# Kernel optimization log

Measured on AMD Instinct MI355X. Metric: run time of the kernel, lower is better.

## Reference

```python
import jax, jax.numpy as jnp
import numpy as np

B, N, L = 16, 512, 512          # batch, compound atoms, protein words
DIM = 10                         # compound feature dim
DM, H, DK, DFF = 128, 8, 16, 512 # transformer dims
LG, LO = 3, 3                    # layer_gnn, layer_output
NFP, NW = 10000, 10000           # vocab sizes
NEG = -9e15                      # GAT mask sentinel (matches torch code)


def _layernorm(x, g, b, eps=1e-6):
    # annotated-transformer LayerNorm: unbiased std, eps added to std
    m = jnp.mean(x, -1, keepdims=True)
    s = jnp.std(x, -1, keepdims=True, ddof=1)
    return g * (x - m) / (s + eps) + b


def _pos_encoding(length, d_model):
    pos = np.arange(length)[:, None]
    div = np.exp(np.arange(0, d_model, 2) * (-np.log(10000.0) / d_model))
    pe = np.zeros((length, d_model), np.float32)
    pe[:, 0::2] = np.sin(pos * div)
    pe[:, 1::2] = np.cos(pos * div)
    return jnp.asarray(pe)


def setup_inputs():
    ks = iter(jax.random.split(jax.random.key(0), 64))
    def nrm(shape, scale):
        return jax.random.normal(next(ks), shape, jnp.float32) * scale
    return dict(
        fingerprints=jax.random.randint(next(ks), (B, N), 0, NFP, jnp.int32),
        fp_mask=jnp.ones((B, N), jnp.float32),
        adjacency=jax.random.randint(next(ks), (B, N, N), 0, 2, jnp.int32),
        words=jax.random.randint(next(ks), (B, L), 0, NW, jnp.int32),
        words_mask=jnp.ones((B, L), jnp.float32),
        emb_fp=nrm((NFP, DIM), 0.1),
        emb_word=nrm((NW, DM), 0.1),
        Wg=nrm((LG, DIM, DIM), 0.3), bg=jnp.zeros((LG, DIM), jnp.float32),
        attn_a=nrm((LG, 2 * DIM), 0.3),
        Wq=nrm((DM, DM), 0.09), bq=jnp.zeros((DM,), jnp.float32),
        Wk=nrm((DM, DM), 0.09), bk=jnp.zeros((DM,), jnp.float32),
        Wv=nrm((DM, DM), 0.09), bv=jnp.zeros((DM,), jnp.float32),
        Wo=nrm((DM, DM), 0.09), bo=jnp.zeros((DM,), jnp.float32),
        ln1_g=jnp.ones((DM,), jnp.float32), ln1_b=jnp.zeros((DM,), jnp.float32),
        ln2_g=jnp.ones((DM,), jnp.float32), ln2_b=jnp.zeros((DM,), jnp.float32),
        lnf_g=jnp.ones((DM,), jnp.float32), lnf_b=jnp.zeros((DM,), jnp.float32),
        W1=nrm((DM, DFF), 0.09), b1=jnp.zeros((DFF,), jnp.float32),
        W2=nrm((DFF, DM), 0.045), b2=jnp.zeros((DM,), jnp.float32),
        Wtout=nrm((DM, DIM), 0.09), btout=jnp.zeros((DIM,), jnp.float32),
        Watt=nrm((DIM, DIM), 0.3), batt=jnp.zeros((DIM,), jnp.float32),
        Wout=nrm((LO, 2 * DIM, 2 * DIM), 0.2), bout=jnp.zeros((LO, 2 * DIM), jnp.float32),
        Wint=nrm((2 * DIM, 2), 0.2), bint=jnp.zeros((2,), jnp.float32),
    )


def _forward(fingerprints, fp_mask, adjacency, words, words_mask,
             emb_fp, emb_word, Wg, bg, attn_a,
             Wq, bq, Wk, bk, Wv, bv, Wo, bo,
             ln1_g, ln1_b, ln2_g, ln2_b, lnf_g, lnf_b,
             W1, b1, W2, b2, Wtout, btout,
             Watt, batt, Wout, bout, Wint, bint):
    # ---- GAT over compound graph (dropout disabled = eval/deterministic) ----
    xs = emb_fp[fingerprints]                     # [B,N,DIM]
    mask = fp_mask[:, :, None]                    # [B,N,1]
    adj = adjacency > 0
    for i in range(LG):
        h = jax.nn.relu(xs @ Wg[i] + bg[i]) * mask
        # e[b,i,j] = leaky_relu(a1.h_i + a2.h_j)  == leaky_relu([h_i||h_j] @ a)
        s1 = h @ attn_a[i, :DIM]                  # [B,N]
        s2 = h @ attn_a[i, DIM:]                  # [B,N]
        e = jax.nn.leaky_relu(s1[:, :, None] + s2[:, None, :])  # [B,N,N]
        att = jax.nn.softmax(jnp.where(adj, e, NEG), axis=2)
        xs = xs + att @ h
    compound = jnp.mean(xs * mask, axis=1, keepdims=True)       # [B,1,DIM]

    # ---- transformer encoder, 1 layer, annotated-transformer (pre-norm) ----
    x = emb_word[words] * jnp.sqrt(jnp.float32(DM)) + _pos_encoding(L, DM)
    m4 = words_mask[:, None, None, :] > 0         # [B,1,1,L]
    xn = _layernorm(x, ln1_g, ln1_b)
    heads = lambda t: t.reshape(B, L, H, DK).transpose(0, 2, 1, 3)
    q, k, v = heads(xn @ Wq + bq), heads(xn @ Wk + bk), heads(xn @ Wv + bv)
    scores = jnp.einsum('bhqd,bhkd->bhqk', q, k) / jnp.sqrt(jnp.float32(DK))
    p = jax.nn.softmax(jnp.where(m4, scores, -1e9), axis=-1)
    attn = jnp.einsum('bhqk,bhkd->bhqd', p, v).transpose(0, 2, 1, 3).reshape(B, L, DM)
    x = x + (attn @ Wo + bo)
    xn = _layernorm(x, ln2_g, ln2_b)
    x = x + (jax.nn.relu(xn @ W1 + b1) @ W2 + b2)
    x = _layernorm(x, lnf_g, lnf_b)
    word_vectors = jax.nn.relu(x) @ Wtout + btout  # [B,L,DIM]

    # ---- tanh cross-attention (attention_cnn) ----
    hc = jax.nn.relu(compound @ Watt + batt)       # [B,1,DIM]
    hp = jax.nn.relu(word_vectors @ Watt + batt)   # [B,L,DIM]
    w = jnp.tanh(jnp.einsum('bxd,bld->bxl', hc, hp))  # [B,1,L]
    protein = jnp.mean(w.transpose(0, 2, 1) * hp, axis=1, keepdims=True)  # [B,1,DIM]

    cat = jnp.concatenate([compound, protein], axis=2)  # [B,1,2*DIM]
    for j in range(LO):
        cat = jax.nn.relu(cat @ Wout[j] + bout[j])
    return jnp.squeeze(cat @ Wint + bint, axis=1)        # [B,2]


def reference(fingerprints, fp_mask, adjacency, words, words_mask,
              emb_fp, emb_word, Wg, bg, attn_a,
              Wq, bq, Wk, bk, Wv, bv, Wo, bo,
              ln1_g, ln1_b, ln2_g, ln2_b, lnf_g, lnf_b,
              W1, b1, W2, b2, Wtout, btout,
              Watt, batt, Wout, bout, Wint, bint):
    return _forward(fingerprints, fp_mask, adjacency, words, words_mask,
                    emb_fp, emb_word, Wg, bg, attn_a,
                    Wq, bq, Wk, bk, Wv, bv, Wo, bo,
                    ln1_g, ln1_b, ln2_g, ln2_b, lnf_g, lnf_b,
                    W1, b1, W2, b2, Wtout, btout,
                    Watt, batt, Wout, bout, Wint, bint)
```

## Files before the change

kernel.cpp:

```cpp
#include <hip/hip_runtime.h>
#include <hip/hip_bf16.h>
#include <math.h>

#define B 16
#define N 512
#define L 512
#define DIM 10
#define DM 128
#define H 8
#define DK 16
#define DFF 512
#define LG 3
#define LO 3
#define NEGV -9.0e15f
#define RF 16
#define AQR 64
#define RLOG2E 1.44269504f

__device__ __forceinline__ float wave_reduce_sum(float v) {
    #pragma unroll
    for (int o = 32; o > 0; o >>= 1) v += __shfl_down(v, o, 64);
    return v;
}

__device__ __forceinline__ float quad_sum(float x) {
    int y1 = __builtin_amdgcn_mov_dpp(__float_as_int(x), 0xB1, 0xF, 0xF, true);
    float s = x + __int_as_float(y1);
    int y2 = __builtin_amdgcn_mov_dpp(__float_as_int(s), 0x4E, 0xF, 0xF, true);
    return s + __int_as_float(y2);
}

__device__ __forceinline__ float half_reduce_sum(float v) {
    #pragma unroll
    for (int o = 16; o > 0; o >>= 1) v += __shfl_xor(v, o, 64);
    return v;
}

__device__ __forceinline__ float fast_exp2(float x) {
    return __builtin_amdgcn_exp2f(x);
}


__global__ void k_embed_fp(const int* __restrict__ fing, const float* __restrict__ emb_fp,
                           float* __restrict__ xs) {
    int idx = blockIdx.x * blockDim.x + threadIdx.x;
    if (idx >= B * N * DIM) return;
    int d = idx % DIM;
    int bn = idx / DIM;
    xs[idx] = emb_fp[fing[bn] * DIM + d];
}

__global__ void k_gnn_h(const float* __restrict__ xs, const float* __restrict__ fp_mask,
                        const float* __restrict__ Wg, const float* __restrict__ bg,
                        const float* __restrict__ aatt,
                        float* __restrict__ h, float* __restrict__ s1, float* __restrict__ s2) {
    int bn = blockIdx.x * blockDim.x + threadIdx.x;
    if (bn >= B * N) return;
    float x[DIM];
    #pragma unroll
    for (int d = 0; d < DIM; d++) x[d] = xs[bn * DIM + d];
    float m = fp_mask[bn];
    float a1 = 0.f, a2 = 0.f;
    #pragma unroll
    for (int j = 0; j < DIM; j++) {
        float acc = bg[j];
        #pragma unroll
        for (int d = 0; d < DIM; d++) acc += x[d] * Wg[d * DIM + j];
        acc = fmaxf(acc, 0.f) * m;
        h[bn * DIM + j] = acc;
        a1 += acc * aatt[j];
        a2 += acc * aatt[DIM + j];
    }
    s1[bn] = a1;
    s2[bn] = a2;
}

__global__ void k_gnn_att(const float* __restrict__ h, const float* __restrict__ s1,
                          const float* __restrict__ s2, const int* __restrict__ adj,
                          float* __restrict__ xs) {
    int b  = blockIdx.x / (N / 16);
    int rg = blockIdx.x % (N / 16);
    int t = threadIdx.x;
    int g  = t >> 4;
    int ll = t & 15;
    int i = rg * 16 + g;

    __shared__ float h_s[N * DIM];
    __shared__ float s2_s[N];

    const float* hb = h + (long)b * N * DIM;
    for (int idx = t; idx < N * DIM; idx += 256) h_s[idx] = hb[idx];
    for (int j = t; j < N; j += 256) s2_s[j] = s2[b * N + j];
    __syncthreads();

    float s1v = s1[b * N + i];
    const int* adjrow = adj + ((long)b * N + i) * N;

    float sum = 0.f;
    float a[DIM];
    #pragma unroll
    for (int d = 0; d < DIM; d++) a[d] = 0.f;
    #pragma unroll
    for (int c = 0; c < 32; c++) {
        int j = c * 16 + ll;
        float xsc = s1v + s2_s[j];
        xsc = xsc > 0.f ? xsc : 0.01f * xsc;
        float e = (adjrow[j] > 0) ? xsc : NEGV;
        float p = fast_exp2(e * RLOG2E);
        sum += p;
        #pragma unroll
        for (int d = 0; d < DIM; d++) a[d] += p * h_s[j * DIM + d];
    }
    #pragma unroll
    for (int off = 1; off < 16; off <<= 1) {
        sum += __shfl_xor(sum, off, 64);
        #pragma unroll
        for (int d = 0; d < DIM; d++) a[d] += __shfl_xor(a[d], off, 64);
    }
    if (ll < DIM) {
        float av = a[0];
        if (ll == 1) av = a[1]; else if (ll == 2) av = a[2]; else if (ll == 3) av = a[3];
        else if (ll == 4) av = a[4]; else if (ll == 5) av = a[5]; else if (ll == 6) av = a[6];
        else if (ll == 7) av = a[7]; else if (ll == 8) av = a[8]; else if (ll == 9) av = a[9];
        xs[((long)b * N + i) * DIM + ll] += av / sum;
    }
}

__global__ void k_compound(const float* __restrict__ xs, const float* __restrict__ fp_mask,
                           const float* __restrict__ Watt, const float* __restrict__ batt,
                           float* __restrict__ compound, float* __restrict__ hc) {
    int b = blockIdx.x;
    int t = threadIdx.x;
    int wid = t >> 6, lane = t & 63;
    float lacc[DIM];
    #pragma unroll
    for (int d = 0; d < DIM; d++) lacc[d] = 0.f;
    for (int n = t; n < N; n += 256) {
        float m = fp_mask[b * N + n];
        #pragma unroll
        for (int d = 0; d < DIM; d++) lacc[d] += xs[((long)b * N + n) * DIM + d] * m;
    }
    __shared__ float red[4][DIM];
    __shared__ float comp_s[DIM];
    #pragma unroll
    for (int d = 0; d < DIM; d++) lacc[d] = wave_reduce_sum(lacc[d]);
    if (lane == 0) {
        #pragma unroll
        for (int d = 0; d < DIM; d++) red[wid][d] = lacc[d];
    }
    __syncthreads();
    if (t < DIM) {
        float c = (red[0][t] + red[1][t] + red[2][t] + red[3][t]) / (float)N;
        compound[b * DIM + t] = c;
        comp_s[t] = c;
    }
    __syncthreads();
    if (t < DIM) {
        float acc = batt[t];
        #pragma unroll
        for (int e = 0; e < DIM; e++) acc += comp_s[e] * Watt[e * DIM + t];
        hc[b * DIM + t] = fmaxf(acc, 0.f);
    }
}


__global__ void k_pe(float* __restrict__ pe) {
    int idx = blockIdx.x * blockDim.x + threadIdx.x;
    if (idx >= L * DM) return;
    int d = idx % DM, l = idx / DM;
    int k = d >> 1;
    double div = exp((double)(2 * k) * (-log(10000.0) / (double)DM));
    double ang = (double)l * div;
    pe[idx] = (d & 1) ? (float)cos(ang) : (float)sin(ang);
}

__global__ void k_embed_ln(const int* __restrict__ words, const float* __restrict__ emb,
                           const float* __restrict__ pe, const float* __restrict__ g,
                           const float* __restrict__ bb,
                           float* __restrict__ x, float* __restrict__ xn) {
    int row = blockIdx.x;
    int t = threadIdx.x;
    int wid = t >> 6, lane = t & 63;
    int l = row % L;
    float v = emb[(long)words[row] * DM + t] * sqrtf(128.0f) + pe[l * DM + t];
    x[(long)row * DM + t] = v;
    float s = wave_reduce_sum(v);
    __shared__ float r2[2], r3[2];
    if (lane == 0) r2[wid] = s;
    __syncthreads();
    float mean = (r2[0] + r2[1]) / (float)DM;
    float dv = v - mean;
    float q = wave_reduce_sum(dv * dv);
    if (lane == 0) r3[wid] = q;
    __syncthreads();
    float sd = sqrtf((r3[0] + r3[1]) / (float)(DM - 1)) + 1e-6f;
    xn[(long)row * DM + t] = g[t] * dv / sd + bb[t];
}

__global__ void k_qkv(const float* __restrict__ xn,
                      const float* __restrict__ Wq, const float* __restrict__ bq,
                      const float* __restrict__ Wk, const float* __restrict__ bk,
                      const float* __restrict__ Wv, const float* __restrict__ bv,
                      float* __restrict__ q, float* __restrict__ k, float* __restrict__ v) {
    long row0 = (long)blockIdx.x * RF;
    int t = threadIdx.x;
    __shared__ float xs_s[RF * DM];
    for (int i = t; i < RF * DM; i += 384) xs_s[i] = xn[row0 * DM + i];
    __syncthreads();
    int proj = t / DM;
    int j = t % DM;
    const float* W    = proj == 0 ? Wq : (proj == 1 ? Wk : Wv);
    const float* bias = proj == 0 ? bq : (proj == 1 ? bk : bv);
    float* out        = proj == 0 ? q  : (proj == 1 ? k  : v);
    float acc[RF];
    #pragma unroll
    for (int r = 0; r < RF; r++) acc[r] = bias[j];
    for (int d4 = 0; d4 < DM / 4; d4++) {
        float w0 = W[(4 * d4 + 0) * DM + j];
        float w1 = W[(4 * d4 + 1) * DM + j];
        float w2 = W[(4 * d4 + 2) * DM + j];
        float w3 = W[(4 * d4 + 3) * DM + j];
        #pragma unroll
        for (int r = 0; r < RF; r++) {
            float4 xv = ((const float4*)&xs_s[r * DM])[d4];
            acc[r] += xv.x * w0 + xv.y * w1 + xv.z * w2 + xv.w * w3;
        }
    }
    #pragma unroll
    for (int r = 0; r < RF; r++) {
        long row = row0 + r;
        int b = (int)(row / L), l = (int)(row % L);
        out[(((long)b * H + j / DK) * L + l) * DK + (j % DK)] = acc[r];
    }
}

__global__ void __launch_bounds__(256, 4)
k_attn(const float* __restrict__ q, const float* __restrict__ k,
       const float* __restrict__ v, const float* __restrict__ wmask,
       float* __restrict__ attnout) {
    int blk = blockIdx.x;
    int qc = blk % (L / AQR);
    int bh = blk / (L / AQR);
    int b = bh / H, hh = bh % H;
    int t = threadIdx.x;
    int sl = t & 3;
    int r = t >> 2;
    int l = qc * AQR + r;

    __shared__ float4 k_s[L * 4];
    __shared__ float wm_s[L];
    const float4* kb4 = (const float4*)(k + (long)bh * L * DK);
    for (int i = t; i < L * 4; i += 256) k_s[i] = kb4[i];
    for (int j = t; j < L; j += 256) wm_s[j] = (wmask[b * L + j] > 0.f) ? 0.f : -1.443e9f;
    __syncthreads();

    float4 qr = ((const float4*)(q + ((long)bh * L + l) * DK))[sl];
    const float qsc = 0.25f * RLOG2E;
    qr.x *= qsc; qr.y *= qsc; qr.z *= qsc; qr.w *= qsc;

    const float4* vb4 = (const float4*)(v + (long)bh * L * DK);

    float ssum = 0.f;
    float4 acc = make_float4(0.f, 0.f, 0.f, 0.f);

    for (int c = 0; c < L / 8; c++) {
        int j0 = c * 8;
        float s8[8];
        #pragma unroll
        for (int jj = 0; jj < 8; jj++) {
            float4 kk = k_s[(j0 + jj) * 4 + sl];
            float part = qr.x * kk.x + qr.y * kk.y + qr.z * kk.z + qr.w * kk.w;
            s8[jj] = quad_sum(part);
        }
        const float4* mp = (const float4*)&wm_s[j0];
        float4 ma = mp[0], mb = mp[1];
        s8[0] += ma.x; s8[1] += ma.y; s8[2] += ma.z; s8[3] += ma.w;
        s8[4] += mb.x; s8[5] += mb.y; s8[6] += mb.z; s8[7] += mb.w;

        #pragma unroll
        for (int jj = 0; jj < 8; jj++) {
            float p = fast_exp2(s8[jj]);
            ssum += p;
            float4 vv = vb4[(j0 + jj) * 4 + sl];
            acc.x += p * vv.x; acc.y += p * vv.y; acc.z += p * vv.z; acc.w += p * vv.w;
        }
    }

    float inv = 1.f / ssum;
    float4* outp = (float4*)(attnout + ((long)b * L + l) * DM + hh * DK);
    outp[sl] = make_float4(acc.x * inv, acc.y * inv, acc.z * inv, acc.w * inv);
}

__global__ void k_oproj(const float* __restrict__ attnout, const float* __restrict__ Wo,
                        const float* __restrict__ bo, float* __restrict__ x) {
    long row0 = (long)blockIdx.x * RF;
    int t = threadIdx.x;
    __shared__ float a_s[RF * DM];
    for (int i = t; i < RF * DM; i += 128) a_s[i] = attnout[row0 * DM + i];
    __syncthreads();
    float acc[RF];
    #pragma unroll
    for (int r = 0; r < RF; r++) acc[r] = bo[t];
    for (int d4 = 0; d4 < DM / 4; d4++) {
        float w0 = Wo[(4 * d4 + 0) * DM + t];
        float w1 = Wo[(4 * d4 + 1) * DM + t];
        float w2 = Wo[(4 * d4 + 2) * DM + t];
        float w3 = Wo[(4 * d4 + 3) * DM + t];
        #pragma unroll
        for (int r = 0; r < RF; r++) {
            float4 av = ((const float4*)&a_s[r * DM])[d4];
            acc[r] += av.x * w0 + av.y * w1 + av.z * w2 + av.w * w3;
        }
    }
    #pragma unroll
    for (int r = 0; r < RF; r++) x[(row0 + r) * DM + t] += acc[r];
}

__global__ void k_ffn_fused(const float* __restrict__ x,
                            const float* __restrict__ ln2_g, const float* __restrict__ ln2_b,
                            const float* __restrict__ W1, const float* __restrict__ b1,
                            const float* __restrict__ W2, const float* __restrict__ b2,
                            const float* __restrict__ lnf_g, const float* __restrict__ lnf_b,
                            const float* __restrict__ Wtout, const float* __restrict__ btout,
                            const float* __restrict__ Watt, const float* __restrict__ batt,
                            float* __restrict__ hp) {
    long row0 = (long)blockIdx.x * RF;
    int t = threadIdx.x;

    __shared__ float x_s[RF][DM];
    __shared__ float xn_s[RF][DM];
    __shared__ float h_s[RF][DFF];
    __shared__ float r_s[RF][DM + 4];
    __shared__ float wt_s[DM * DIM];
    __shared__ float wa_s[DIM * DIM];
    __shared__ float bt_s[DIM], ba_s[DIM];
    __shared__ float wv_s[RF][DIM];

    {
        float4 xv = ((const float4*)(x + row0 * DM))[t];
        ((float4*)&x_s[0][0])[t] = xv;
        for (int i = t; i < DM * DIM; i += 512) wt_s[i] = Wtout[i];
        for (int i = t; i < DIM * DIM; i += 512) wa_s[i] = Watt[i];
        if (t < DIM) { bt_s[t] = btout[t]; ba_s[t] = batt[t]; }
    }
    __syncthreads();

    {
        int row = t >> 5, c = t & 31;
        float4 v = ((const float4*)&x_s[row][0])[c];
        float s = half_reduce_sum(v.x + v.y + v.z + v.w);
        float mean = s / (float)DM;
        float4 dv = make_float4(v.x - mean, v.y - mean, v.z - mean, v.w - mean);
        float q = half_reduce_sum(dv.x * dv.x + dv.y * dv.y + dv.z * dv.z + dv.w * dv.w);
        float sd = sqrtf(q / (float)(DM - 1)) + 1e-6f;
        const float4 g4 = ((const float4*)ln2_g)[c];
        const float4 b4 = ((const float4*)ln2_b)[c];
        ((float4*)&xn_s[row][0])[c] = make_float4(
            g4.x * dv.x / sd + b4.x, g4.y * dv.y / sd + b4.y,
            g4.z * dv.z / sd + b4.z, g4.w * dv.w / sd + b4.w);
    }
    __syncthreads();

    {
        float acc[RF];
        #pragma unroll
        for (int r = 0; r < RF; r++) acc[r] = b1[t];
        for (int d4 = 0; d4 < DM / 4; d4++) {
            float w0 = W1[(4 * d4 + 0) * DFF + t];
            float w1 = W1[(4 * d4 + 1) * DFF + t];
            float w2 = W1[(4 * d4 + 2) * DFF + t];
            float w3 = W1[(4 * d4 + 3) * DFF + t];
            #pragma unroll
            for (int r = 0; r < RF; r++) {
                float4 xv = ((const float4*)&xn_s[r][0])[d4];
                acc[r] += xv.x * w0 + xv.y * w1 + xv.z * w2 + xv.w * w3;
            }
        }
        #pragma unroll
        for (int r = 0; r < RF; r++) h_s[r][t] = fmaxf(acc[r], 0.f);
    }
    __syncthreads();

    {
        int col = t & 127, rq = t >> 7;
        float acc2[4];
        #pragma unroll
        for (int rr = 0; rr < 4; rr++) acc2[rr] = b2[col];
        for (int f4 = 0; f4 < DFF / 4; f4++) {
            float w0 = W2[(4 * f4 + 0) * DM + col];
            float w1 = W2[(4 * f4 + 1) * DM + col];
            float w2 = W2[(4 * f4 + 2) * DM + col];
            float w3 = W2[(4 * f4 + 3) * DM + col];
            #pragma unroll
            for (int rr = 0; rr < 4; rr++) {
                float4 hv = ((const float4*)&h_s[rq * 4 + rr][0])[f4];
                acc2[rr] += hv.x * w0 + hv.y * w1 + hv.z * w2 + hv.w * w3;
            }
        }
        __syncthreads();
        #pragma unroll
        for (int rr = 0; rr < 4; rr++) {
            int row = rq * 4 + rr;
            xn_s[row][col] = x_s[row][col] + acc2[rr];
        }
    }
    __syncthreads();

    {
        int row = t >> 5, c = t & 31;
        float4 v = ((const float4*)&xn_s[row][0])[c];
        float s = half_reduce_sum(v.x + v.y + v.z + v.w);
        float mean = s / (float)DM;
        float4 dv = make_float4(v.x - mean, v.y - mean, v.z - mean, v.w - mean);
        float q = half_reduce_sum(dv.x * dv.x + dv.y * dv.y + dv.z * dv.z + dv.w * dv.w);
        float sd = sqrtf(q / (float)(DM - 1)) + 1e-6f;
        const float4 g4 = ((const float4*)lnf_g)[c];
        const float4 b4 = ((const float4*)lnf_b)[c];
        r_s[row][4 * c + 0] = fmaxf(g4.x * dv.x / sd + b4.x, 0.f);
        r_s[row][4 * c + 1] = fmaxf(g4.y * dv.y / sd + b4.y, 0.f);
        r_s[row][4 * c + 2] = fmaxf(g4.z * dv.z / sd + b4.z, 0.f);
        r_s[row][4 * c + 3] = fmaxf(g4.w * dv.w / sd + b4.w, 0.f);
    }
    __syncthreads();

    if (t < RF * DIM) {
        int row = t / DIM, o = t % DIM;
        float acc = bt_s[o];
        for (int d = 0; d < DM; d++) acc += r_s[row][d] * wt_s[d * DIM + o];
        wv_s[row][o] = acc;
    }
    __syncthreads();

    if (t < RF * DIM) {
        int row = t / DIM, o = t % DIM;
        float acc = ba_s[o];
        #pragma unroll
        for (int e = 0; e < DIM; e++) acc += wv_s[row][e] * wa_s[e * DIM + o];
        hp[(row0 + row) * DIM + o] = fmaxf(acc, 0.f);
    }
}

__global__ void k_final(const float* __restrict__ hp, const float* __restrict__ hc,
                        const float* __restrict__ compound, const float* __restrict__ Wout,
                        const float* __restrict__ bout, const float* __restrict__ Wint,
                        const float* __restrict__ bint, float* __restrict__ out) {
    int b = blockIdx.x;
    int t = threadIdx.x;
    int wid = t >> 6, lane = t & 63;

    __shared__ float wout_s[LO * 2 * DIM * 2 * DIM];
    __shared__ float bout_s[LO * 2 * DIM];
    __shared__ float wint_s[2 * DIM * 2];
    __shared__ float bint_s[2];
    __shared__ float hc_s[DIM];
    __shared__ float red[4][DIM];
    __shared__ float cat_s[2 * DIM];
    __shared__ float tmp_s[2 * DIM];

    for (int i = t; i < LO * 2 * DIM * 2 * DIM; i += 256) wout_s[i] = Wout[i];
    for (int i = t; i < LO * 2 * DIM; i += 256) bout_s[i] = bout[i];
    for (int i = t; i < 2 * DIM * 2; i += 256) wint_s[i] = Wint[i];
    if (t < 2) bint_s[t] = bint[t];
    if (t < DIM) hc_s[t] = hc[b * DIM + t];
    __syncthreads();

    float lacc[DIM];
    #pragma unroll
    for (int e = 0; e < DIM; e++) lacc[e] = 0.f;
    for (int l = t; l < L; l += 256) {
        const float* hpl = hp + ((long)b * L + l) * DIM;
        float hv[DIM];
        float dot = 0.f;
        #pragma unroll
        for (int e = 0; e < DIM; e++) { hv[e] = hpl[e]; dot += hc_s[e] * hv[e]; }
        float w = tanhf(dot);
        #pragma unroll
        for (int e = 0; e < DIM; e++) lacc[e] += w * hv[e];
    }
    #pragma unroll
    for (int e = 0; e < DIM; e++) lacc[e] = wave_reduce_sum(lacc[e]);
    if (lane == 0) {
        #pragma unroll
        for (int e = 0; e < DIM; e++) red[wid][e] = lacc[e];
    }
    __syncthreads();
    if (t < DIM) {
        cat_s[t] = compound[b * DIM + t];
        cat_s[DIM + t] = (red[0][t] + red[1][t] + red[2][t] + red[3][t]) / (float)L;
    }
    __syncthreads();

    for (int j = 0; j < LO; j++) {
        float acc = 0.f;
        if (t < 2 * DIM) {
            acc = bout_s[j * 2 * DIM + t];
            #pragma unroll
            for (int e = 0; e < 2 * DIM; e++)
                acc += cat_s[e] * wout_s[j * 2 * DIM * 2 * DIM + e * 2 * DIM + t];
            acc = fmaxf(acc, 0.f);
            tmp_s[t] = acc;
        }
        __syncthreads();
        if (t < 2 * DIM) cat_s[t] = tmp_s[t];
        __syncthreads();
    }
    if (t < 2) {
        float o = bint_s[t];
        #pragma unroll
        for (int e = 0; e < 2 * DIM; e++) o += cat_s[e] * wint_s[e * 2 + t];
        out[b * 2 + t] = o;
    }
}

extern "C" void kernel_launch(void* const* d_in, const int* in_sizes, int n_in,
                              void* d_out, int out_size, void* d_ws, size_t ws_size,
                              hipStream_t stream) {
    (void)in_sizes; (void)n_in; (void)out_size; (void)ws_size;
    const int*   fingerprints = (const int*)d_in[0];
    const float* fp_mask      = (const float*)d_in[1];
    const int*   adjacency    = (const int*)d_in[2];
    const int*   words        = (const int*)d_in[3];
    const float* words_mask   = (const float*)d_in[4];
    const float* emb_fp       = (const float*)d_in[5];
    const float* emb_word     = (const float*)d_in[6];
    const float* Wg   = (const float*)d_in[7];
    const float* bg   = (const float*)d_in[8];
    const float* attn_a = (const float*)d_in[9];
    const float* Wq = (const float*)d_in[10];
    const float* bq = (const float*)d_in[11];
    const float* Wk = (const float*)d_in[12];
    const float* bk = (const float*)d_in[13];
    const float* Wv = (const float*)d_in[14];
    const float* bv = (const float*)d_in[15];
    const float* Wo = (const float*)d_in[16];
    const float* bo = (const float*)d_in[17];
    const float* ln1_g = (const float*)d_in[18];
    const float* ln1_b = (const float*)d_in[19];
    const float* ln2_g = (const float*)d_in[20];
    const float* ln2_b = (const float*)d_in[21];
    const float* lnf_g = (const float*)d_in[22];
    const float* lnf_b = (const float*)d_in[23];
    const float* W1 = (const float*)d_in[24];
    const float* b1 = (const float*)d_in[25];
    const float* W2 = (const float*)d_in[26];
    const float* b2 = (const float*)d_in[27];
    const float* Wtout = (const float*)d_in[28];
    const float* btout = (const float*)d_in[29];
    const float* Watt  = (const float*)d_in[30];
    const float* batt  = (const float*)d_in[31];
    const float* Wout  = (const float*)d_in[32];
    const float* bout  = (const float*)d_in[33];
    const float* Wint  = (const float*)d_in[34];
    const float* bint  = (const float*)d_in[35];
    float* out = (float*)d_out;

    float* w = (float*)d_ws;
    float* xs = w;        w += B * N * DIM;
    float* h  = w;        w += B * N * DIM;
    float* s1 = w;        w += B * N;
    float* s2 = w;        w += B * N;
    float* compound = w;  w += B * DIM;
    float* hc = w;        w += B * DIM;
    float* pe = w;        w += L * DM;
    float* x  = w;        w += (long)B * L * DM;
    float* xn = w;        w += (long)B * L * DM;
    float* qb = w;        w += (long)B * H * L * DK;
    float* kb = w;        w += (long)B * H * L * DK;
    float* vb = w;        w += (long)B * H * L * DK;
    float* attnout = w;   w += (long)B * L * DM;
    float* hp = w;        w += (long)B * L * DIM;

    k_embed_fp<<<(B * N * DIM + 255) / 256, 256, 0, stream>>>(fingerprints, emb_fp, xs);
    for (int i = 0; i < LG; i++) {
        k_gnn_h<<<(B * N + 255) / 256, 256, 0, stream>>>(
            xs, fp_mask, Wg + i * DIM * DIM, bg + i * DIM, attn_a + i * 2 * DIM, h, s1, s2);
        k_gnn_att<<<B * (N / 16), 256, 0, stream>>>(h, s1, s2, adjacency, xs);
    }
    k_compound<<<B, 256, 0, stream>>>(xs, fp_mask, Watt, batt, compound, hc);

    k_pe<<<(L * DM + 255) / 256, 256, 0, stream>>>(pe);
    k_embed_ln<<<B * L, DM, 0, stream>>>(words, emb_word, pe, ln1_g, ln1_b, x, xn);
    k_qkv<<<B * L / RF, 3 * DM, 0, stream>>>(xn, Wq, bq, Wk, bk, Wv, bv, qb, kb, vb);
    k_attn<<<B * H * (L / AQR), 256, 0, stream>>>(qb, kb, vb, words_mask, attnout);
    k_oproj<<<B * L / RF, DM, 0, stream>>>(attnout, Wo, bo, x);
    k_ffn_fused<<<B * L / RF, DFF, 0, stream>>>(x, ln2_g, ln2_b, W1, b1, W2, b2,
                                                lnf_g, lnf_b, Wtout, btout, Watt, batt, hp);
    k_final<<<B, 256, 0, stream>>>(hp, hc, compound, Wout, bout, Wint, bint, out);
}
```

Before: 237.9 us.

## Split attention keys into two segments and merge partial sums in output projection

Attention blocks now each cover half of the key range (split-K), doubling the grid, and write unnormalised partial outputs plus row sums. The output projection then combines the two partials and normalises them. Separately, the fingerprint-embedding kernel is folded into the first GNN layer and the positional-encoding kernel is folded into the word-embedding LayerNorm kernel. The aim is more parallelism in attention and fewer launches, at the cost of extra partial-buffer traffic and per-thread double-precision sin/cos in the embedding kernel. The merge is valid only because the scores are never max-subtracted, so the softmax sums across segments combine directly.

```diff
diff --git a/kernel.cpp b/kernel.cpp
--- a/kernel.cpp
+++ b/kernel.cpp
@@ -15,6 +15,7 @@
 #define NEGV -9.0e15f
 #define RF 16
 #define AQR 64
+#define KSEG 256
 #define RLOG2E 1.44269504f
 
 __device__ __forceinline__ float wave_reduce_sum(float v) {
@@ -41,24 +42,23 @@
 }
 
 
-__global__ void k_embed_fp(const int* __restrict__ fing, const float* __restrict__ emb_fp,
-                           float* __restrict__ xs) {
-    int idx = blockIdx.x * blockDim.x + threadIdx.x;
-    if (idx >= B * N * DIM) return;
-    int d = idx % DIM;
-    int bn = idx / DIM;
-    xs[idx] = emb_fp[fing[bn] * DIM + d];
-}
-
-__global__ void k_gnn_h(const float* __restrict__ xs, const float* __restrict__ fp_mask,
+__global__ void k_gnn_h(const int* __restrict__ fing, const float* __restrict__ emb_fp,
+                        float* __restrict__ xs, const float* __restrict__ fp_mask,
                         const float* __restrict__ Wg, const float* __restrict__ bg,
                         const float* __restrict__ aatt,
-                        float* __restrict__ h, float* __restrict__ s1, float* __restrict__ s2) {
+                        float* __restrict__ h, float* __restrict__ s1, float* __restrict__ s2,
+                        int first) {
     int bn = blockIdx.x * blockDim.x + threadIdx.x;
     if (bn >= B * N) return;
     float x[DIM];
-    #pragma unroll
-    for (int d = 0; d < DIM; d++) x[d] = xs[bn * DIM + d];
+    if (first) {
+        long base = (long)fing[bn] * DIM;
+        #pragma unroll
+        for (int d = 0; d < DIM; d++) { x[d] = emb_fp[base + d]; xs[bn * DIM + d] = x[d]; }
+    } else {
+        #pragma unroll
+        for (int d = 0; d < DIM; d++) x[d] = xs[bn * DIM + d];
+    }
     float m = fp_mask[bn];
     float a1 = 0.f, a2 = 0.f;
     #pragma unroll
@@ -164,25 +164,18 @@
 }
 
 
-__global__ void k_pe(float* __restrict__ pe) {
-    int idx = blockIdx.x * blockDim.x + threadIdx.x;
-    if (idx >= L * DM) return;
-    int d = idx % DM, l = idx / DM;
-    int k = d >> 1;
-    double div = exp((double)(2 * k) * (-log(10000.0) / (double)DM));
-    double ang = (double)l * div;
-    pe[idx] = (d & 1) ? (float)cos(ang) : (float)sin(ang);
-}
-
 __global__ void k_embed_ln(const int* __restrict__ words, const float* __restrict__ emb,
-                           const float* __restrict__ pe, const float* __restrict__ g,
-                           const float* __restrict__ bb,
+                           const float* __restrict__ g, const float* __restrict__ bb,
                            float* __restrict__ x, float* __restrict__ xn) {
     int row = blockIdx.x;
     int t = threadIdx.x;
     int wid = t >> 6, lane = t & 63;
     int l = row % L;
-    float v = emb[(long)words[row] * DM + t] * sqrtf(128.0f) + pe[l * DM + t];
+    int k2 = (t >> 1) * 2;
+    double div = exp((double)k2 * (-log(10000.0) / (double)DM));
+    double ang = (double)l * div;
+    float pev = (t & 1) ? (float)cos(ang) : (float)sin(ang);
+    float v = emb[(long)words[row] * DM + t] * sqrtf(128.0f) + pev;
     x[(long)row * DM + t] = v;
     float s = wave_reduce_sum(v);
     __shared__ float r2[2], r3[2];
@@ -237,33 +230,37 @@
 __global__ void __launch_bounds__(256, 4)
 k_attn(const float* __restrict__ q, const float* __restrict__ k,
        const float* __restrict__ v, const float* __restrict__ wmask,
-       float* __restrict__ attnout) {
+       float* __restrict__ attn_p, float* __restrict__ ssum_p) {
     int blk = blockIdx.x;
-    int qc = blk % (L / AQR);
-    int bh = blk / (L / AQR);
+    int seg = blk & 1;
+    int rest = blk >> 1;
+    int qc = rest % (L / AQR);
+    int bh = rest / (L / AQR);
     int b = bh / H, hh = bh % H;
     int t = threadIdx.x;
     int sl = t & 3;
     int r = t >> 2;
     int l = qc * AQR + r;
-
-    __shared__ float4 k_s[L * 4];
-    __shared__ float wm_s[L];
-    const float4* kb4 = (const float4*)(k + (long)bh * L * DK);
-    for (int i = t; i < L * 4; i += 256) k_s[i] = kb4[i];
-    for (int j = t; j < L; j += 256) wm_s[j] = (wmask[b * L + j] > 0.f) ? 0.f : -1.443e9f;
+    int j00 = seg * KSEG;
+
+    __shared__ float4 k_s[KSEG * 4];
+    __shared__ float wm_s[KSEG];
+    const float4* kb4 = (const float4*)(k + (long)bh * L * DK) + (long)j00 * 4;
+    for (int i = t; i < KSEG * 4; i += 256) k_s[i] = kb4[i];
+    for (int j = t; j < KSEG; j += 256)
+        wm_s[j] = (wmask[b * L + j00 + j] > 0.f) ? 0.f : -1.443e9f;
     __syncthreads();
 
     float4 qr = ((const float4*)(q + ((long)bh * L + l) * DK))[sl];
     const float qsc = 0.25f * RLOG2E;
     qr.x *= qsc; qr.y *= qsc; qr.z *= qsc; qr.w *= qsc;
 
-    const float4* vb4 = (const float4*)(v + (long)bh * L * DK);
+    const float4* vb4 = (const float4*)(v + (long)bh * L * DK) + (long)j00 * 4;
 
     float ssum = 0.f;
     float4 acc = make_float4(0.f, 0.f, 0.f, 0.f);
 
-    for (int c = 0; c < L / 8; c++) {
+    for (int c = 0; c < KSEG / 8; c++) {
         int j0 = c * 8;
         float s8[8];
         #pragma unroll
@@ -286,18 +283,42 @@
         }
     }
 
-    float inv = 1.f / ssum;
-    float4* outp = (float4*)(attnout + ((long)b * L + l) * DM + hh * DK);
-    outp[sl] = make_float4(acc.x * inv, acc.y * inv, acc.z * inv, acc.w * inv);
-}
-
-__global__ void k_oproj(const float* __restrict__ attnout, const float* __restrict__ Wo,
-                        const float* __restrict__ bo, float* __restrict__ x) {
+    float4* outp = (float4*)(attn_p + (((long)seg * B + b) * L + l) * DM + hh * DK);
+    outp[sl] = acc;
+    if (sl == 0) ssum_p[(((long)seg * B + b) * H + hh) * L + l] = ssum;
+}
+
+__global__ void k_oproj(const float* __restrict__ attn_p, const float* __restrict__ ssum_p,
+                        const float* __restrict__ Wo, const float* __restrict__ bo,
+                        float* __restrict__ x) {
     long row0 = (long)blockIdx.x * RF;
     int t = threadIdx.x;
+    int b = (int)(row0 / L);
+    int l0 = (int)(row0 % L);
+
     __shared__ float a_s[RF * DM];
-    for (int i = t; i < RF * DM; i += 128) a_s[i] = attnout[row0 * DM + i];
-    __syncthreads();
+    __shared__ float inv_s[RF][H];
+
+    {
+        int row = t >> 3, hh = t & 7;
+        float s0 = ssum_p[(((long)0 * B + b) * H + hh) * L + (l0 + row)];
+        float s1 = ssum_p[(((long)1 * B + b) * H + hh) * L + (l0 + row)];
+        inv_s[row][hh] = 1.f / (s0 + s1);
+    }
+    __syncthreads();
+
+    const float4* p0 = (const float4*)(attn_p + (((long)0 * B + b) * L + l0) * DM);
+    const float4* p1 = (const float4*)(attn_p + (((long)1 * B + b) * L + l0) * DM);
+    for (int i = t; i < RF * DM / 4; i += 128) {
+        float4 a0 = p0[i], a1 = p1[i];
+        int row = i >> 5;
+        int hh = (i & 31) >> 2;
+        float inv = inv_s[row][hh];
+        ((float4*)a_s)[i] = make_float4((a0.x + a1.x) * inv, (a0.y + a1.y) * inv,
+                                        (a0.z + a1.z) * inv, (a0.w + a1.w) * inv);
+    }
+    __syncthreads();
+
     float acc[RF];
     #pragma unroll
     for (int r = 0; r < RF; r++) acc[r] = bo[t];
@@ -561,28 +582,27 @@
     float* s2 = w;        w += B * N;
     float* compound = w;  w += B * DIM;
     float* hc = w;        w += B * DIM;
-    float* pe = w;        w += L * DM;
     float* x  = w;        w += (long)B * L * DM;
     float* xn = w;        w += (long)B * L * DM;
     float* qb = w;        w += (long)B * H * L * DK;
     float* kb = w;        w += (long)B * H * L * DK;
     float* vb = w;        w += (long)B * H * L * DK;
-    float* attnout = w;   w += (long)B * L * DM;
+    float* attn_p = w;    w += 2L * B * L * DM;
+    float* ssum_p = w;    w += 2L * B * H * L;
     float* hp = w;        w += (long)B * L * DIM;
 
-    k_embed_fp<<<(B * N * DIM + 255) / 256, 256, 0, stream>>>(fingerprints, emb_fp, xs);
     for (int i = 0; i < LG; i++) {
         k_gnn_h<<<(B * N + 255) / 256, 256, 0, stream>>>(
-            xs, fp_mask, Wg + i * DIM * DIM, bg + i * DIM, attn_a + i * 2 * DIM, h, s1, s2);
+            fingerprints, emb_fp, xs, fp_mask,
+            Wg + i * DIM * DIM, bg + i * DIM, attn_a + i * 2 * DIM, h, s1, s2, i == 0);
         k_gnn_att<<<B * (N / 16), 256, 0, stream>>>(h, s1, s2, adjacency, xs);
     }
     k_compound<<<B, 256, 0, stream>>>(xs, fp_mask, Watt, batt, compound, hc);
 
-    k_pe<<<(L * DM + 255) / 256, 256, 0, stream>>>(pe);
-    k_embed_ln<<<B * L, DM, 0, stream>>>(words, emb_word, pe, ln1_g, ln1_b, x, xn);
+    k_embed_ln<<<B * L, DM, 0, stream>>>(words, emb_word, ln1_g, ln1_b, x, xn);
     k_qkv<<<B * L / RF, 3 * DM, 0, stream>>>(xn, Wq, bq, Wk, bk, Wv, bv, qb, kb, vb);
-    k_attn<<<B * H * (L / AQR), 256, 0, stream>>>(qb, kb, vb, words_mask, attnout);
-    k_oproj<<<B * L / RF, DM, 0, stream>>>(attnout, Wo, bo, x);
+    k_attn<<<B * H * (L / AQR) * 2, 256, 0, stream>>>(qb, kb, vb, words_mask, attn_p, ssum_p);
+    k_oproj<<<B * L / RF, DM, 0, stream>>>(attn_p, ssum_p, Wo, bo, x);
     k_ffn_fused<<<B * L / RF, DFF, 0, stream>>>(x, ln2_g, ln2_b, W1, b1, W2, b2,
                                                 lnf_g, lnf_b, Wtout, btout, Watt, batt, hp);
     k_final<<<B, 256, 0, stream>>>(hp, hc, compound, Wout, bout, Wint, bint, out);
```

After: 232.3 us. 2.4% less time.
